# Optimization experiments

Hardware: AMD Instinct MI355X
Metric: run time of the kernel (lower is better)

## Reference

```python
import jax, jax.numpy as jnp
import numpy as np

EPS = 1e-5
NUM_GROUPS = 32
NUM_HEADS = 4


def setup_inputs() -> dict:
    key = jax.random.key(0)
    ks = jax.random.split(key, 3)
    B, C, H, W = 4, 256, 64, 64
    x = jax.random.normal(ks[0], (B, C, H, W), dtype=jnp.float32)
    gn_w = jnp.ones((C,), jnp.float32)
    gn_b = jnp.zeros((C,), jnp.float32)
    qkv_w = jax.random.normal(ks[1], (3 * C, C), dtype=jnp.float32) * (C ** -0.5)
    qkv_b = jnp.zeros((3 * C,), jnp.float32)
    proj_w = jax.random.normal(ks[2], (C, C), dtype=jnp.float32) * (C ** -0.5)
    proj_b = jnp.zeros((C,), jnp.float32)
    return {"x": x, "gn_w": gn_w, "gn_b": gn_b, "qkv_w": qkv_w,
            "qkv_b": qkv_b, "proj_w": proj_w, "proj_b": proj_b}


def _group_norm(x, w, b):
    B, C, H, W = x.shape
    xg = x.reshape(B, NUM_GROUPS, C // NUM_GROUPS, H, W)
    mean = xg.mean(axis=(2, 3, 4), keepdims=True)
    var = xg.var(axis=(2, 3, 4), keepdims=True)
    xn = ((xg - mean) * jax.lax.rsqrt(var + EPS)).reshape(B, C, H, W)
    return xn * w[None, :, None, None] + b[None, :, None, None]


def reference(x, gn_w, gn_b, qkv_w, qkv_b, proj_w, proj_b):
    B, C, H, W = x.shape
    nh = NUM_HEADS
    d = C // nh
    L = H * W
    h = _group_norm(x, gn_w, gn_b)
    # 1x1 conv == channel matmul
    qkv = jnp.einsum('oc,bchw->bohw', qkv_w, h) + qkv_b[None, :, None, None]
    q, k, v = jnp.split(qkv, 3, axis=1)
    # (B, C, H, W) -> (B, nh, L, d)
    def to_heads(t):
        return t.reshape(B, nh, d, L).transpose(0, 1, 3, 2)
    q, k, v = to_heads(q), to_heads(k), to_heads(v)
    scale = d ** -0.5
    attn = jax.nn.softmax(jnp.einsum('bhqd,bhkd->bhqk', q, k) * scale, axis=-1)
    o = jnp.einsum('bhqk,bhkd->bhqd', attn, v)          # (B, nh, L, d)
    o = o.transpose(0, 1, 3, 2).reshape(B, C, H, W)
    o = jnp.einsum('oc,bchw->bohw', proj_w, o) + proj_b[None, :, None, None]
    return x + o
```

## Files before the change

### kernel.cpp

```cpp
#include <hip/hip_runtime.h>

#define B_   4
#define C_   256
#define L_   4096
#define NH_  4
#define D_   64
#define G_   32
#define CPG_ 8

typedef __bf16 bf16x8 __attribute__((ext_vector_type(8)));
typedef float  f32x4  __attribute__((ext_vector_type(4)));

__device__ __forceinline__ ushort f2bf(float f) {
  union { float f; unsigned u; } c; c.f = f;
  unsigned u = c.u;
  return (ushort)((u + 0x7fffu + ((u >> 16) & 1u)) >> 16);
}
__device__ __forceinline__ float bf2f(ushort h) {
  union { unsigned u; float f; } c; c.u = ((unsigned)h) << 16; return c.f;
}
__device__ __forceinline__ unsigned fbits(float f) {
  union { float f; unsigned u; } c; c.f = f; return c.u;
}
__device__ __forceinline__ float fastexp2(float x) {
#if __has_builtin(__builtin_amdgcn_exp2f)
  return __builtin_amdgcn_exp2f(x);
#else
  return exp2f(x);
#endif
}

__global__ __launch_bounds__(256) void cvt_kernel(const float* __restrict__ wq,
                                                  const float* __restrict__ wp,
                                                  ushort* __restrict__ oq,
                                                  ushort* __restrict__ op,
                                                  float* __restrict__ stats) {
  int t = blockIdx.x * 256 + threadIdx.x;
  if (blockIdx.x == 0) stats[threadIdx.x] = 0.f;
  const int NQ4 = (768 * 256) / 4;
  float4 v;
  if (t < NQ4) {
    v = ((const float4*)wq)[t];
    ((ushort4*)oq)[t] = make_ushort4(f2bf(v.x), f2bf(v.y), f2bf(v.z), f2bf(v.w));
  } else {
    int i = t - NQ4;
    v = ((const float4*)wp)[i];
    ((ushort4*)op)[i] = make_ushort4(f2bf(v.x), f2bf(v.y), f2bf(v.z), f2bf(v.w));
  }
}

__global__ __launch_bounds__(256) void gn_stats(const float* __restrict__ x,
                                                float* __restrict__ stats) {
  int bg = blockIdx.x >> 3, chunk = blockIdx.x & 7;
  int b = bg >> 5, g = bg & 31;
  const float* xg = x + ((size_t)b * C_ + g * CPG_) * L_ + chunk * 512;
  int tid = threadIdx.x;

  float s = 0.f, ss = 0.f;
  for (int c = 0; c < CPG_; ++c) {
    float2 v = ((const float2*)(xg + (size_t)c * L_))[tid];
    s  += v.x + v.y;
    ss += v.x * v.x + v.y * v.y;
  }
  for (int off = 32; off; off >>= 1) { s += __shfl_xor(s, off); ss += __shfl_xor(ss, off); }
  __shared__ float red[8];
  int w = tid >> 6;
  if ((tid & 63) == 0) { red[w] = s; red[4 + w] = ss; }
  __syncthreads();
  if (tid == 0) {
    atomicAdd(&stats[bg * 2],     red[0] + red[1] + red[2] + red[3]);
    atomicAdd(&stats[bg * 2 + 1], red[4] + red[5] + red[6] + red[7]);
  }
}

__global__ __launch_bounds__(256) void gn_apply(const float* __restrict__ x,
                                                const float* __restrict__ gw,
                                                const float* __restrict__ gb,
                                                const float* __restrict__ stats,
                                                ushort* __restrict__ hT) {
  int bg = blockIdx.x >> 3, chunk = blockIdx.x & 7;
  int b = bg >> 5, g = bg & 31;
  const float* xg = x + ((size_t)b * C_ + g * CPG_) * L_;
  int tid = threadIdx.x;

  const float inv_n = 1.0f / (CPG_ * L_);
  float mean = stats[bg * 2] * inv_n;
  float var  = stats[bg * 2 + 1] * inv_n - mean * mean;
  float rstd = rsqrtf(var + 1e-5f);

  float wv[CPG_], bv[CPG_];
  for (int c = 0; c < CPG_; ++c) { wv[c] = gw[g * CPG_ + c]; bv[c] = gb[g * CPG_ + c]; }

  for (int li = 0; li < 2; ++li) {
    int l = chunk * 512 + li * 256 + tid;
    union { ushort s[8]; uint4 u; } o;
    for (int c = 0; c < CPG_; ++c) {
      float v = xg[(size_t)c * L_ + l];
      o.s[c] = f2bf((v - mean) * rstd * wv[c] + bv[c]);
    }
    *(uint4*)(hT + ((size_t)b * L_ + l) * C_ + g * CPG_) = o.u;
  }
}

__global__ __launch_bounds__(256) void qkv_kernel(const ushort* __restrict__ hT,
                                                  const ushort* __restrict__ w,
                                                  const float* __restrict__ bias,
                                                  ushort* __restrict__ q,
                                                  ushort* __restrict__ k,
                                                  ushort* __restrict__ v) {
  int wid  = blockIdx.x * 4 + (threadIdx.x >> 6);
  int lane = threadIdx.x & 63;
  int quad = lane >> 4, col = lane & 15;
  int ot   = wid % 12;
  int rest = wid / 12;
  int lt   = rest & 127;
  int b    = rest >> 7;
  int o0 = ot * 64, l0 = lt * 32;

  const ushort* abase = w  + (size_t)(o0 + col) * C_ + quad * 8;
  const ushort* bbase = hT + ((size_t)b * L_ + l0 + col) * C_ + quad * 8;

  f32x4 acc[4][2];
  for (int i = 0; i < 4; ++i) for (int j = 0; j < 2; ++j)
    acc[i][j] = (f32x4){0.f, 0.f, 0.f, 0.f};

  for (int k0 = 0; k0 < C_; k0 += 32) {
    bf16x8 a[4], bb[2];
#pragma unroll
    for (int i = 0; i < 4; ++i) a[i]  = *(const bf16x8*)(abase + (size_t)(i * 16) * C_ + k0);
#pragma unroll
    for (int j = 0; j < 2; ++j) bb[j] = *(const bf16x8*)(bbase + (size_t)(j * 16) * C_ + k0);
#pragma unroll
    for (int i = 0; i < 4; ++i)
#pragma unroll
      for (int j = 0; j < 2; ++j)
        acc[i][j] = __builtin_amdgcn_mfma_f32_16x16x32_bf16(a[i], bb[j], acc[i][j], 0, 0, 0);
  }

  int third = o0 >> 8;
  int hh    = (o0 & 255) >> 6;
  float scale = (third == 0) ? 0.180336880111120f : 1.0f;
#pragma unroll
  for (int i = 0; i < 4; ++i) {
    int oo = o0 + i * 16 + quad * 4;
    int dd = i * 16 + quad * 4;
#pragma unroll
    for (int j = 0; j < 2; ++j) {
      int l = l0 + j * 16 + col;
      ushort pk[4];
      for (int r = 0; r < 4; ++r) pk[r] = f2bf((acc[i][j][r] + bias[oo + r]) * scale);
      if (third < 2) {
        ushort* dst = (third ? k : q) + (((size_t)(b * NH_ + hh) * L_ + l) * D_ + dd);
        *(ushort4*)dst = make_ushort4(pk[0], pk[1], pk[2], pk[3]);
      } else {
        for (int r = 0; r < 4; ++r)
          v[((size_t)(b * NH_ + hh) * D_ + dd + r) * L_ + l] = pk[r];
      }
    }
  }
}

__global__ __launch_bounds__(256) void attn_kernel(const ushort* __restrict__ q,
                                                   const ushort* __restrict__ k,
                                                   const ushort* __restrict__ v,
                                                   ushort* __restrict__ p0,
                                                   ushort* __restrict__ p1,
                                                   float* __restrict__ psumbuf) {
  __shared__ __align__(16) ushort k_lds[64][72];
  __shared__ __align__(16) ushort v_lds[64][72];

  int tid   = threadIdx.x;
  int w     = tid >> 6, lane = tid & 63;
  int quad  = lane >> 4, col = lane & 15;
  int split = blockIdx.x >> 9;
  int bh    = (blockIdx.x >> 5) & 15;
  int qblk  = blockIdx.x & 31;

  const ushort* qp = q + (size_t)bh * L_ * D_;
  const ushort* kp = k + (size_t)bh * L_ * D_;
  const ushort* vp = v + (size_t)bh * D_ * L_;

  int qrow0 = qblk * 128 + w * 32;
  bf16x8 bq[2][2];
#pragma unroll
  for (int f = 0; f < 2; ++f)
#pragma unroll
    for (int c = 0; c < 2; ++c)
      bq[f][c] = *(const bf16x8*)(qp + (size_t)(qrow0 + f * 16 + col) * D_ + c * 32 + quad * 8);

  f32x4 oacc[2][4];
#pragma unroll
  for (int f = 0; f < 2; ++f)
    for (int t = 0; t < 4; ++t) oacc[f][t] = (f32x4){0.f, 0.f, 0.f, 0.f};
  float psum[2] = {0.f, 0.f};

  int vrow = tid >> 2, vchunk = tid & 3;
  int kt0 = split * (L_ / 2);

  for (int kt = kt0; kt < kt0 + L_ / 2; kt += 64) {
    __syncthreads();
    {
      const uint4* ksrc = (const uint4*)(kp + (size_t)kt * D_);
      uint4 k0 = ksrc[tid];
      uint4 k1 = ksrc[tid + 256];
      *(uint4*)&k_lds[tid >> 3][(tid & 7) * 8] = k0;
      *(uint4*)&k_lds[32 + (tid >> 3)][(tid & 7) * 8] = k1;
      const uint4* vsrc = (const uint4*)(vp + (size_t)vrow * L_ + kt);
      uint4 v0 = vsrc[vchunk * 2];
      uint4 v1 = vsrc[vchunk * 2 + 1];
      *(uint4*)&v_lds[vrow][vchunk * 16] = v0;
      *(uint4*)&v_lds[vrow][vchunk * 16 + 8] = v1;
    }
    __syncthreads();

#pragma unroll
    for (int h = 0; h < 2; ++h) {
      f32x4 s0[2], s1[2];
#pragma unroll
      for (int f = 0; f < 2; ++f) { s0[f] = (f32x4){0.f,0.f,0.f,0.f}; s1[f] = (f32x4){0.f,0.f,0.f,0.f}; }
#pragma unroll
      for (int c = 0; c < 2; ++c) {
        bf16x8 a0 = *(const bf16x8*)&k_lds[h * 32 + col][c * 32 + quad * 8];
        bf16x8 a1 = *(const bf16x8*)&k_lds[h * 32 + 16 + col][c * 32 + quad * 8];
#pragma unroll
        for (int f = 0; f < 2; ++f) {
          s0[f] = __builtin_amdgcn_mfma_f32_16x16x32_bf16(a0, bq[f][c], s0[f], 0, 0, 0);
          s1[f] = __builtin_amdgcn_mfma_f32_16x16x32_bf16(a1, bq[f][c], s1[f], 0, 0, 0);
        }
      }

      bf16x8 pb[2];
#pragma unroll
      for (int f = 0; f < 2; ++f) {
        float pe0[4], pe1[4];
#pragma unroll
        for (int r = 0; r < 4; ++r) {
          pe0[r] = fastexp2(s0[f][r]);
          pe1[r] = fastexp2(s1[f][r]);
          psum[f] += pe0[r] + pe1[r];
        }
        union { unsigned u[4]; bf16x8 v8; } pc;
        pc.u[0] = __builtin_amdgcn_perm(fbits(pe0[1]), fbits(pe0[0]), 0x07060302u);
        pc.u[1] = __builtin_amdgcn_perm(fbits(pe0[3]), fbits(pe0[2]), 0x07060302u);
        pc.u[2] = __builtin_amdgcn_perm(fbits(pe1[1]), fbits(pe1[0]), 0x07060302u);
        pc.u[3] = __builtin_amdgcn_perm(fbits(pe1[3]), fbits(pe1[2]), 0x07060302u);
        pb[f] = pc.v8;
      }

#pragma unroll
      for (int t = 0; t < 4; ++t) {
        union { uint2 u2[2]; bf16x8 v8; } vc;
        vc.u2[0] = *(const uint2*)&v_lds[t * 16 + col][h * 32 + quad * 4];
        vc.u2[1] = *(const uint2*)&v_lds[t * 16 + col][h * 32 + 16 + quad * 4];
        bf16x8 av = vc.v8;
#pragma unroll
        for (int f = 0; f < 2; ++f)
          oacc[f][t] = __builtin_amdgcn_mfma_f32_16x16x32_bf16(av, pb[f], oacc[f][t], 0, 0, 0);
      }
    }
  }

  ushort* po = split ? p1 : p0;
#pragma unroll
  for (int f = 0; f < 2; ++f) {
    psum[f] += __shfl_xor(psum[f], 16);
    psum[f] += __shfl_xor(psum[f], 32);
    for (int t = 0; t < 4; ++t) {
      ushort ok[4];
      for (int r = 0; r < 4; ++r) ok[r] = f2bf(oacc[f][t][r]);
      ushort* dst = po + ((size_t)bh * L_ + qrow0 + f * 16 + col) * D_ + t * 16 + quad * 4;
      *(ushort4*)dst = make_ushort4(ok[0], ok[1], ok[2], ok[3]);
    }
    if (quad == 0)
      psumbuf[split * (16 * L_) + bh * L_ + qrow0 + f * 16 + col] = psum[f];
  }
}

__global__ __launch_bounds__(256) void comb_kernel(ushort* __restrict__ p0,
                                                   const ushort* __restrict__ p1,
                                                   const float* __restrict__ ps) {
  int idx = blockIdx.x * 256 + threadIdx.x;
  int row = idx >> 4;
  float inv = 1.0f / (ps[row] + ps[16 * L_ + row]);
  ushort4 a = ((const ushort4*)p0)[idx];
  ushort4 b = ((const ushort4*)p1)[idx];
  ((ushort4*)p0)[idx] = make_ushort4(
      f2bf((bf2f(a.x) + bf2f(b.x)) * inv),
      f2bf((bf2f(a.y) + bf2f(b.y)) * inv),
      f2bf((bf2f(a.z) + bf2f(b.z)) * inv),
      f2bf((bf2f(a.w) + bf2f(b.w)) * inv));
}

__global__ __launch_bounds__(256) void proj_kernel(const ushort* __restrict__ oin,
                                                   const ushort* __restrict__ pw,
                                                   const float* __restrict__ pb,
                                                   const float* __restrict__ x,
                                                   float* __restrict__ out) {
  int wid  = blockIdx.x * 4 + (threadIdx.x >> 6);
  int lane = threadIdx.x & 63;
  int quad = lane >> 4, col = lane & 15;
  int oct  = wid & 7;
  int rest = wid >> 3;
  int lt   = rest & 127;
  int b    = rest >> 7;
  int l0 = lt * 32, oc0 = oct * 32;

  f32x4 acc[2][2];
  for (int i = 0; i < 2; ++i) for (int j = 0; j < 2; ++j)
    acc[i][j] = (f32x4){0.f, 0.f, 0.f, 0.f};

  for (int k0 = 0; k0 < C_; k0 += 32) {
    int hh = k0 >> 6, dk = k0 & 63;
    bf16x8 a[2], bb[2];
#pragma unroll
    for (int i = 0; i < 2; ++i)
      a[i] = *(const bf16x8*)(oin + ((size_t)(b * NH_ + hh) * L_ + l0 + i * 16 + col) * D_ + dk + quad * 8);
#pragma unroll
    for (int j = 0; j < 2; ++j)
      bb[j] = *(const bf16x8*)(pw + (size_t)(oc0 + j * 16 + col) * C_ + k0 + quad * 8);
#pragma unroll
    for (int i = 0; i < 2; ++i)
#pragma unroll
      for (int j = 0; j < 2; ++j)
        acc[i][j] = __builtin_amdgcn_mfma_f32_16x16x32_bf16(a[i], bb[j], acc[i][j], 0, 0, 0);
  }

#pragma unroll
  for (int j = 0; j < 2; ++j) {
    int oc = oc0 + j * 16 + col;
    float bias = pb[oc];
#pragma unroll
    for (int i = 0; i < 2; ++i) {
      int l = l0 + i * 16 + quad * 4;
      size_t off = ((size_t)b * C_ + oc) * L_ + l;
      float4 xv = *(const float4*)(x + off);
      float4 ov = make_float4(acc[i][j][0] + bias + xv.x,
                              acc[i][j][1] + bias + xv.y,
                              acc[i][j][2] + bias + xv.z,
                              acc[i][j][3] + bias + xv.w);
      *(float4*)(out + off) = ov;
    }
  }
}

extern "C" void kernel_launch(void* const* d_in, const int* in_sizes, int n_in,
                              void* d_out, int out_size, void* d_ws, size_t ws_size,
                              hipStream_t stream) {
  const float* x      = (const float*)d_in[0];
  const float* gn_w   = (const float*)d_in[1];
  const float* gn_b   = (const float*)d_in[2];
  const float* qkv_w  = (const float*)d_in[3];
  const float* qkv_b  = (const float*)d_in[4];
  const float* proj_w = (const float*)d_in[5];
  const float* proj_b = (const float*)d_in[6];
  float* out = (float*)d_out;

  const size_t TEN = (size_t)B_ * C_ * L_;
  ushort* ws  = (ushort*)d_ws;
  ushort* q   = ws;
  ushort* k   = ws + TEN;
  ushort* v   = ws + 2 * TEN;
  ushort* oat = ws + 3 * TEN;
  ushort* wq  = ws + 4 * TEN;
  ushort* wp  = wq + 768 * 256;
  float*  stats = (float*)(wp + 256 * 256);
  ushort* hT  = (ushort*)d_out;
  ushort* p1  = (ushort*)d_out + TEN;
  float*  psb = (float*)d_out;

  cvt_kernel <<<256,       256, 0, stream>>>(qkv_w, proj_w, wq, wp, stats);
  gn_stats   <<<1024,      256, 0, stream>>>(x, stats);
  gn_apply   <<<1024,      256, 0, stream>>>(x, gn_w, gn_b, stats, hT);
  qkv_kernel <<<6144 / 4,  256, 0, stream>>>(hT, wq, qkv_b, q, k, v);
  attn_kernel<<<1024,      256, 0, stream>>>(q, k, v, oat, p1, psb);
  comb_kernel<<<4096,      256, 0, stream>>>(oat, p1, psb);
  proj_kernel<<<4096 / 4,  256, 0, stream>>>(oat, wp, proj_b, x, out);
}
```

Measured before the change: 236.5 us.

## Double-buffer K/V tiles in attention and compute row sums via MFMA

The attention kernel now double-buffers K and V in shared memory, issuing global loads for the next tile before the current tile's compute and storing them afterward, which drops one barrier per iteration and overlaps memory latency with MFMA work. The softmax denominator is now accumulated with an extra MFMA against a vector of ones instead of scalar adds and shuffles. It also adds s_setprio hints around the MFMA sections and an occupancy hint in launch_bounds. The cost is doubled LDS usage and more live registers for the prefetched data. The row sums now come from the bf16-rounded probabilities rather than the fp32 values.

```diff
diff --git a/kernel.cpp b/kernel.cpp
--- a/kernel.cpp
+++ b/kernel.cpp
@@ -160,14 +160,14 @@
   }
 }
 
-__global__ __launch_bounds__(256) void attn_kernel(const ushort* __restrict__ q,
-                                                   const ushort* __restrict__ k,
-                                                   const ushort* __restrict__ v,
-                                                   ushort* __restrict__ p0,
-                                                   ushort* __restrict__ p1,
-                                                   float* __restrict__ psumbuf) {
-  __shared__ __align__(16) ushort k_lds[64][72];
-  __shared__ __align__(16) ushort v_lds[64][72];
+__global__ __launch_bounds__(256, 4) void attn_kernel(const ushort* __restrict__ q,
+                                                      const ushort* __restrict__ k,
+                                                      const ushort* __restrict__ v,
+                                                      ushort* __restrict__ p0,
+                                                      ushort* __restrict__ p1,
+                                                      float* __restrict__ psumbuf) {
+  __shared__ __align__(16) ushort k_lds[2][64][72];
+  __shared__ __align__(16) ushort v_lds[2][64][72];
 
   int tid   = threadIdx.x;
   int w     = tid >> 6, lane = tid & 63;
@@ -192,42 +192,62 @@
 #pragma unroll
   for (int f = 0; f < 2; ++f)
     for (int t = 0; t < 4; ++t) oacc[f][t] = (f32x4){0.f, 0.f, 0.f, 0.f};
-  float psum[2] = {0.f, 0.f};
+  f32x4 pacc[2];
+  pacc[0] = (f32x4){0.f, 0.f, 0.f, 0.f};
+  pacc[1] = (f32x4){0.f, 0.f, 0.f, 0.f};
+
+  union { ushort s[8]; bf16x8 v8; } one_u;
+#pragma unroll
+  for (int i = 0; i < 8; ++i) one_u.s[i] = 0x3F80;
+  bf16x8 ones = one_u.v8;
 
   int vrow = tid >> 2, vchunk = tid & 3;
-  int kt0 = split * (L_ / 2);
-
-  for (int kt = kt0; kt < kt0 + L_ / 2; kt += 64) {
-    __syncthreads();
-    {
-      const uint4* ksrc = (const uint4*)(kp + (size_t)kt * D_);
-      uint4 k0 = ksrc[tid];
-      uint4 k1 = ksrc[tid + 256];
-      *(uint4*)&k_lds[tid >> 3][(tid & 7) * 8] = k0;
-      *(uint4*)&k_lds[32 + (tid >> 3)][(tid & 7) * 8] = k1;
-      const uint4* vsrc = (const uint4*)(vp + (size_t)vrow * L_ + kt);
-      uint4 v0 = vsrc[vchunk * 2];
-      uint4 v1 = vsrc[vchunk * 2 + 1];
-      *(uint4*)&v_lds[vrow][vchunk * 16] = v0;
-      *(uint4*)&v_lds[vrow][vchunk * 16 + 8] = v1;
-    }
-    __syncthreads();
+  int kt0 = split * (L_ / 2), kt_end = kt0 + L_ / 2;
+
+  {
+    const uint4* ksrc = (const uint4*)(kp + (size_t)kt0 * D_);
+    uint4 a  = ksrc[tid];
+    uint4 b2 = ksrc[tid + 256];
+    const uint4* vsrc = (const uint4*)(vp + (size_t)vrow * L_ + kt0);
+    uint4 c0 = vsrc[vchunk * 2];
+    uint4 c1 = vsrc[vchunk * 2 + 1];
+    *(uint4*)&k_lds[0][tid >> 3][(tid & 7) * 8] = a;
+    *(uint4*)&k_lds[0][32 + (tid >> 3)][(tid & 7) * 8] = b2;
+    *(uint4*)&v_lds[0][vrow][vchunk * 16] = c0;
+    *(uint4*)&v_lds[0][vrow][vchunk * 16 + 8] = c1;
+  }
+  __syncthreads();
+
+  int cur = 0;
+  for (int kt = kt0; kt < kt_end; kt += 64) {
+    uint4 nk0, nk1, nv0, nv1;
+    bool has_next = (kt + 64) < kt_end;
+    if (has_next) {
+      const uint4* ksrc = (const uint4*)(kp + (size_t)(kt + 64) * D_);
+      nk0 = ksrc[tid];
+      nk1 = ksrc[tid + 256];
+      const uint4* vsrc = (const uint4*)(vp + (size_t)vrow * L_ + (kt + 64));
+      nv0 = vsrc[vchunk * 2];
+      nv1 = vsrc[vchunk * 2 + 1];
+    }
 
 #pragma unroll
     for (int h = 0; h < 2; ++h) {
       f32x4 s0[2], s1[2];
 #pragma unroll
       for (int f = 0; f < 2; ++f) { s0[f] = (f32x4){0.f,0.f,0.f,0.f}; s1[f] = (f32x4){0.f,0.f,0.f,0.f}; }
+      __builtin_amdgcn_s_setprio(1);
 #pragma unroll
       for (int c = 0; c < 2; ++c) {
-        bf16x8 a0 = *(const bf16x8*)&k_lds[h * 32 + col][c * 32 + quad * 8];
-        bf16x8 a1 = *(const bf16x8*)&k_lds[h * 32 + 16 + col][c * 32 + quad * 8];
+        bf16x8 a0 = *(const bf16x8*)&k_lds[cur][h * 32 + col][c * 32 + quad * 8];
+        bf16x8 a1 = *(const bf16x8*)&k_lds[cur][h * 32 + 16 + col][c * 32 + quad * 8];
 #pragma unroll
         for (int f = 0; f < 2; ++f) {
           s0[f] = __builtin_amdgcn_mfma_f32_16x16x32_bf16(a0, bq[f][c], s0[f], 0, 0, 0);
           s1[f] = __builtin_amdgcn_mfma_f32_16x16x32_bf16(a1, bq[f][c], s1[f], 0, 0, 0);
         }
       }
+      __builtin_amdgcn_s_setprio(0);
 
       bf16x8 pb[2];
 #pragma unroll
@@ -237,7 +257,6 @@
         for (int r = 0; r < 4; ++r) {
           pe0[r] = fastexp2(s0[f][r]);
           pe1[r] = fastexp2(s1[f][r]);
-          psum[f] += pe0[r] + pe1[r];
         }
         union { unsigned u[4]; bf16x8 v8; } pc;
         pc.u[0] = __builtin_amdgcn_perm(fbits(pe0[1]), fbits(pe0[0]), 0x07060302u);
@@ -247,24 +266,37 @@
         pb[f] = pc.v8;
       }
 
+      __builtin_amdgcn_s_setprio(1);
+#pragma unroll
+      for (int f = 0; f < 2; ++f)
+        pacc[f] = __builtin_amdgcn_mfma_f32_16x16x32_bf16(ones, pb[f], pacc[f], 0, 0, 0);
 #pragma unroll
       for (int t = 0; t < 4; ++t) {
         union { uint2 u2[2]; bf16x8 v8; } vc;
-        vc.u2[0] = *(const uint2*)&v_lds[t * 16 + col][h * 32 + quad * 4];
-        vc.u2[1] = *(const uint2*)&v_lds[t * 16 + col][h * 32 + 16 + quad * 4];
+        vc.u2[0] = *(const uint2*)&v_lds[cur][t * 16 + col][h * 32 + quad * 4];
+        vc.u2[1] = *(const uint2*)&v_lds[cur][t * 16 + col][h * 32 + 16 + quad * 4];
         bf16x8 av = vc.v8;
 #pragma unroll
         for (int f = 0; f < 2; ++f)
           oacc[f][t] = __builtin_amdgcn_mfma_f32_16x16x32_bf16(av, pb[f], oacc[f][t], 0, 0, 0);
       }
+      __builtin_amdgcn_s_setprio(0);
+    }
+
+    if (has_next) {
+      int nb = cur ^ 1;
+      *(uint4*)&k_lds[nb][tid >> 3][(tid & 7) * 8] = nk0;
+      *(uint4*)&k_lds[nb][32 + (tid >> 3)][(tid & 7) * 8] = nk1;
+      *(uint4*)&v_lds[nb][vrow][vchunk * 16] = nv0;
+      *(uint4*)&v_lds[nb][vrow][vchunk * 16 + 8] = nv1;
+      __syncthreads();
+      cur = nb;
     }
   }
 
   ushort* po = split ? p1 : p0;
 #pragma unroll
   for (int f = 0; f < 2; ++f) {
-    psum[f] += __shfl_xor(psum[f], 16);
-    psum[f] += __shfl_xor(psum[f], 32);
     for (int t = 0; t < 4; ++t) {
       ushort ok[4];
       for (int r = 0; r < 4; ++r) ok[r] = f2bf(oacc[f][t][r]);
@@ -272,7 +304,7 @@
       *(ushort4*)dst = make_ushort4(ok[0], ok[1], ok[2], ok[3]);
     }
     if (quad == 0)
-      psumbuf[split * (16 * L_) + bh * L_ + qrow0 + f * 16 + col] = psum[f];
+      psumbuf[split * (16 * L_) + bh * L_ + qrow0 + f * 16 + col] = pacc[f][0];
   }
 }
 
```

Result: faster. 225.0 us (-4.9%).

## Software-pipeline attention with double-buffered LDS and QK/softmax-PV overlap

Applied to the files above, without the earlier changes.

Restructures the attention kernel into a software pipeline. LDS is double-buffered, global loads for the next K/V tile are issued before compute, and the QK MMA for tile n+1 is interleaved with softmax and PV for tile n. This removes one barrier per iteration and hides load latency. V is stored in LDS with a permuted layout so each PV fragment is a single 16-byte read. The change also remaps block IDs to spread work, adds an occupancy hint to launch bounds, and fully unrolls the K loops in the QKV and projection GEMMs. The extra live fragments raise register pressure, which could conflict with the requested occupancy of 4.

```diff
diff --git a/kernel.cpp b/kernel.cpp
--- a/kernel.cpp
+++ b/kernel.cpp
@@ -124,6 +124,7 @@
   for (int i = 0; i < 4; ++i) for (int j = 0; j < 2; ++j)
     acc[i][j] = (f32x4){0.f, 0.f, 0.f, 0.f};
 
+#pragma unroll
   for (int k0 = 0; k0 < C_; k0 += 32) {
     bf16x8 a[4], bb[2];
 #pragma unroll
@@ -160,21 +161,23 @@
   }
 }
 
-__global__ __launch_bounds__(256) void attn_kernel(const ushort* __restrict__ q,
-                                                   const ushort* __restrict__ k,
-                                                   const ushort* __restrict__ v,
-                                                   ushort* __restrict__ p0,
-                                                   ushort* __restrict__ p1,
-                                                   float* __restrict__ psumbuf) {
-  __shared__ __align__(16) ushort k_lds[64][72];
-  __shared__ __align__(16) ushort v_lds[64][72];
+__global__ __launch_bounds__(256, 4) void attn_kernel(const ushort* __restrict__ q,
+                                                      const ushort* __restrict__ k,
+                                                      const ushort* __restrict__ v,
+                                                      ushort* __restrict__ p0,
+                                                      ushort* __restrict__ p1,
+                                                      float* __restrict__ psumbuf) {
+  __shared__ __align__(16) ushort k_lds[2][64][72];
+  __shared__ __align__(16) ushort v_lds[2][64][72];
 
   int tid   = threadIdx.x;
   int w     = tid >> 6, lane = tid & 63;
   int quad  = lane >> 4, col = lane & 15;
-  int split = blockIdx.x >> 9;
-  int bh    = (blockIdx.x >> 5) & 15;
-  int qblk  = blockIdx.x & 31;
+  int bid   = (int)blockIdx.x;
+  bid = (bid & 7) * 128 + (bid >> 3);
+  int split = bid >> 9;
+  int bh    = (bid >> 5) & 15;
+  int qblk  = bid & 31;
 
   const ushort* qp = q + (size_t)bh * L_ * D_;
   const ushort* kp = k + (size_t)bh * L_ * D_;
@@ -193,72 +196,138 @@
   for (int f = 0; f < 2; ++f)
     for (int t = 0; t < 4; ++t) oacc[f][t] = (f32x4){0.f, 0.f, 0.f, 0.f};
   float psum[2] = {0.f, 0.f};
+  const f32x4 Z = (f32x4){0.f, 0.f, 0.f, 0.f};
 
   int vrow = tid >> 2, vchunk = tid & 3;
+  int vwoff = (vchunk >> 1) * 32 + (vchunk & 1) * 4;
   int kt0 = split * (L_ / 2);
 
-  for (int kt = kt0; kt < kt0 + L_ / 2; kt += 64) {
+  uint4 gk0, gk1, gv0, gv1;
+  bf16x8 vfA[2][4], vfB[2][4];
+  f32x4  sA[2][2][2], sB[2][2][2];
+  int cur = 0;
+
+#define GLOBAL_ISSUE(KT) { \
+    const uint4* ksrc_ = (const uint4*)(kp + (size_t)(KT) * D_); \
+    gk0 = ksrc_[tid]; \
+    gk1 = ksrc_[tid + 256]; \
+    const uint4* vsrc_ = (const uint4*)(vp + (size_t)vrow * L_ + (KT)); \
+    gv0 = vsrc_[vchunk * 2]; \
+    gv1 = vsrc_[vchunk * 2 + 1]; \
+  }
+
+#define STAGE_WRITE(NB) { \
+    *(uint4*)&k_lds[NB][tid >> 3][(tid & 7) * 8] = gk0; \
+    *(uint4*)&k_lds[NB][32 + (tid >> 3)][(tid & 7) * 8] = gk1; \
+    ushort* vb_ = &v_lds[NB][vrow][vwoff]; \
+    *(uint2*)(vb_ + 0)  = make_uint2(gv0.x, gv0.y); \
+    *(uint2*)(vb_ + 8)  = make_uint2(gv0.z, gv0.w); \
+    *(uint2*)(vb_ + 16) = make_uint2(gv1.x, gv1.y); \
+    *(uint2*)(vb_ + 24) = make_uint2(gv1.z, gv1.w); \
+  }
+
+#define READ_KF(KF) { \
+    _Pragma("unroll") \
+    for (int h = 0; h < 2; ++h) { \
+      KF[h][0][0] = *(const bf16x8*)&k_lds[cur][h * 32 + col][quad * 8]; \
+      KF[h][0][1] = *(const bf16x8*)&k_lds[cur][h * 32 + col][32 + quad * 8]; \
+      KF[h][1][0] = *(const bf16x8*)&k_lds[cur][h * 32 + 16 + col][quad * 8]; \
+      KF[h][1][1] = *(const bf16x8*)&k_lds[cur][h * 32 + 16 + col][32 + quad * 8]; \
+    } \
+  }
+
+#define READ_VF(VF) { \
+    _Pragma("unroll") \
+    for (int h = 0; h < 2; ++h) \
+      _Pragma("unroll") \
+      for (int t = 0; t < 4; ++t) \
+        VF[h][t] = *(const bf16x8*)&v_lds[cur][t * 16 + col][h * 32 + quad * 8]; \
+  }
+
+#define QK_TILE(KF, S) { \
+    _Pragma("unroll") \
+    for (int h = 0; h < 2; ++h) \
+      _Pragma("unroll") \
+      for (int f = 0; f < 2; ++f) { \
+        S[h][f][0] = __builtin_amdgcn_mfma_f32_16x16x32_bf16(KF[h][0][0], bq[f][0], Z, 0, 0, 0); \
+        S[h][f][1] = __builtin_amdgcn_mfma_f32_16x16x32_bf16(KF[h][1][0], bq[f][0], Z, 0, 0, 0); \
+        S[h][f][0] = __builtin_amdgcn_mfma_f32_16x16x32_bf16(KF[h][0][1], bq[f][1], S[h][f][0], 0, 0, 0); \
+        S[h][f][1] = __builtin_amdgcn_mfma_f32_16x16x32_bf16(KF[h][1][1], bq[f][1], S[h][f][1], 0, 0, 0); \
+      } \
+  }
+
+#define SOFT_PV(S, VF) { \
+    _Pragma("unroll") \
+    for (int h = 0; h < 2; ++h) { \
+      bf16x8 pb[2]; \
+      _Pragma("unroll") \
+      for (int f = 0; f < 2; ++f) { \
+        float pe0[4], pe1[4]; \
+        _Pragma("unroll") \
+        for (int r = 0; r < 4; ++r) { \
+          pe0[r] = fastexp2(S[h][f][0][r]); \
+          pe1[r] = fastexp2(S[h][f][1][r]); \
+        } \
+        psum[f] += ((pe0[0] + pe0[1]) + (pe0[2] + pe0[3])) + \
+                   ((pe1[0] + pe1[1]) + (pe1[2] + pe1[3])); \
+        union { unsigned u[4]; bf16x8 v8; } pc; \
+        pc.u[0] = __builtin_amdgcn_perm(fbits(pe0[1]), fbits(pe0[0]), 0x07060302u); \
+        pc.u[1] = __builtin_amdgcn_perm(fbits(pe0[3]), fbits(pe0[2]), 0x07060302u); \
+        pc.u[2] = __builtin_amdgcn_perm(fbits(pe1[1]), fbits(pe1[0]), 0x07060302u); \
+        pc.u[3] = __builtin_amdgcn_perm(fbits(pe1[3]), fbits(pe1[2]), 0x07060302u); \
+        pb[f] = pc.v8; \
+      } \
+      _Pragma("unroll") \
+      for (int t = 0; t < 4; ++t) \
+        _Pragma("unroll") \
+        for (int f = 0; f < 2; ++f) \
+          oacc[f][t] = __builtin_amdgcn_mfma_f32_16x16x32_bf16(VF[h][t], pb[f], oacc[f][t], 0, 0, 0); \
+    } \
+  }
+
+#define BODY(SP, SN, VP, VN, KTNEXT, HASNEXT) { \
+    cur ^= 1; \
+    bf16x8 kf[2][2][2]; \
+    READ_KF(kf); \
+    READ_VF(VN); \
+    if (HASNEXT) GLOBAL_ISSUE(KTNEXT); \
+    QK_TILE(kf, SN); \
+    SOFT_PV(SP, VP); \
+    if (HASNEXT) { STAGE_WRITE(cur ^ 1); __syncthreads(); } \
+  }
+
+  GLOBAL_ISSUE(kt0);
+  STAGE_WRITE(0);
+  __syncthreads();
+
+  {
+    bf16x8 kf[2][2][2];
+    READ_KF(kf);
+    READ_VF(vfA);
+    GLOBAL_ISSUE(kt0 + 64);
+    QK_TILE(kf, sA);
+    STAGE_WRITE(1);
     __syncthreads();
-    {
-      const uint4* ksrc = (const uint4*)(kp + (size_t)kt * D_);
-      uint4 k0 = ksrc[tid];
-      uint4 k1 = ksrc[tid + 256];
-      *(uint4*)&k_lds[tid >> 3][(tid & 7) * 8] = k0;
-      *(uint4*)&k_lds[32 + (tid >> 3)][(tid & 7) * 8] = k1;
-      const uint4* vsrc = (const uint4*)(vp + (size_t)vrow * L_ + kt);
-      uint4 v0 = vsrc[vchunk * 2];
-      uint4 v1 = vsrc[vchunk * 2 + 1];
-      *(uint4*)&v_lds[vrow][vchunk * 16] = v0;
-      *(uint4*)&v_lds[vrow][vchunk * 16 + 8] = v1;
-    }
-    __syncthreads();
-
-#pragma unroll
-    for (int h = 0; h < 2; ++h) {
-      f32x4 s0[2], s1[2];
-#pragma unroll
-      for (int f = 0; f < 2; ++f) { s0[f] = (f32x4){0.f,0.f,0.f,0.f}; s1[f] = (f32x4){0.f,0.f,0.f,0.f}; }
-#pragma unroll
-      for (int c = 0; c < 2; ++c) {
-        bf16x8 a0 = *(const bf16x8*)&k_lds[h * 32 + col][c * 32 + quad * 8];
-        bf16x8 a1 = *(const bf16x8*)&k_lds[h * 32 + 16 + col][c * 32 + quad * 8];
-#pragma unroll
-        for (int f = 0; f < 2; ++f) {
-          s0[f] = __builtin_amdgcn_mfma_f32_16x16x32_bf16(a0, bq[f][c], s0[f], 0, 0, 0);
-          s1[f] = __builtin_amdgcn_mfma_f32_16x16x32_bf16(a1, bq[f][c], s1[f], 0, 0, 0);
-        }
-      }
-
-      bf16x8 pb[2];
-#pragma unroll
-      for (int f = 0; f < 2; ++f) {
-        float pe0[4], pe1[4];
-#pragma unroll
-        for (int r = 0; r < 4; ++r) {
-          pe0[r] = fastexp2(s0[f][r]);
-          pe1[r] = fastexp2(s1[f][r]);
-          psum[f] += pe0[r] + pe1[r];
-        }
-        union { unsigned u[4]; bf16x8 v8; } pc;
-        pc.u[0] = __builtin_amdgcn_perm(fbits(pe0[1]), fbits(pe0[0]), 0x07060302u);
-        pc.u[1] = __builtin_amdgcn_perm(fbits(pe0[3]), fbits(pe0[2]), 0x07060302u);
-        pc.u[2] = __builtin_amdgcn_perm(fbits(pe1[1]), fbits(pe1[0]), 0x07060302u);
-        pc.u[3] = __builtin_amdgcn_perm(fbits(pe1[3]), fbits(pe1[2]), 0x07060302u);
-        pb[f] = pc.v8;
-      }
-
-#pragma unroll
-      for (int t = 0; t < 4; ++t) {
-        union { uint2 u2[2]; bf16x8 v8; } vc;
-        vc.u2[0] = *(const uint2*)&v_lds[t * 16 + col][h * 32 + quad * 4];
-        vc.u2[1] = *(const uint2*)&v_lds[t * 16 + col][h * 32 + 16 + quad * 4];
-        bf16x8 av = vc.v8;
-#pragma unroll
-        for (int f = 0; f < 2; ++f)
-          oacc[f][t] = __builtin_amdgcn_mfma_f32_16x16x32_bf16(av, pb[f], oacc[f][t], 0, 0, 0);
-      }
-    }
-  }
+  }
+
+  for (int j = 0; j < 15; ++j) {
+    int ktn1 = kt0 + (2 * j + 2) * 64;
+    int ktn2 = kt0 + (2 * j + 3) * 64;
+    BODY(sA, sB, vfA, vfB, ktn1, true);
+    BODY(sB, sA, vfB, vfA, ktn2, true);
+  }
+
+  BODY(sA, sB, vfA, vfB, 0, false);
+
+  SOFT_PV(sB, vfB);
+
+#undef BODY
+#undef SOFT_PV
+#undef QK_TILE
+#undef READ_VF
+#undef READ_KF
+#undef STAGE_WRITE
+#undef GLOBAL_ISSUE
 
   ushort* po = split ? p1 : p0;
 #pragma unroll
@@ -309,6 +378,7 @@
   for (int i = 0; i < 2; ++i) for (int j = 0; j < 2; ++j)
     acc[i][j] = (f32x4){0.f, 0.f, 0.f, 0.f};
 
+#pragma unroll
   for (int k0 = 0; k0 < C_; k0 += 32) {
     int hh = k0 >> 6, dk = k0 & 63;
     bf16x8 a[2], bb[2];
```

After: 371.6 us. 1.57x slower.
